# Optimization experiments

Hardware: AMD Instinct MI355X
Metric: run time of the kernel (lower is better)

## Reference

```python
import jax, jax.numpy as jnp
import numpy as np

N_NODES = 50000
N_EDGES = 600000
IN_CH = 128
OUT_CH = 128


def setup_inputs() -> dict:
    key = jax.random.key(0)
    k1, k2, k3, k4 = jax.random.split(key, 4)
    x = jax.random.normal(k1, (N_NODES, IN_CH), dtype=jnp.float32)
    edge_index = jax.random.randint(k2, (2, N_EDGES), 0, N_NODES, dtype=jnp.int64)
    W_msg = jax.random.normal(k3, (OUT_CH, IN_CH * 9), dtype=jnp.float32) * (1.0 / np.sqrt(IN_CH * 9))
    b_msg = jnp.zeros((OUT_CH,), dtype=jnp.float32)
    W_root = jax.random.normal(k4, (OUT_CH, IN_CH), dtype=jnp.float32) * (1.0 / np.sqrt(IN_CH))
    b_root = jnp.zeros((OUT_CH,), dtype=jnp.float32)
    return {"x": x, "edge_index": edge_index, "W_msg": W_msg, "b_msg": b_msg,
            "W_root": W_root, "b_root": b_root}


def reference(x, edge_index, W_msg, b_msg, W_root, b_root):
    n = x.shape[0]
    src = edge_index[0]
    dst = edge_index[1]

    # in-degree per destination node
    degree = jax.ops.segment_sum(jnp.ones_like(dst, dtype=x.dtype), dst, num_segments=n)  # [N]

    msgs = x[src]  # [E, C] gathered source features
    agg_sum = jax.ops.segment_sum(msgs, dst, num_segments=n)                 # [N, C]
    agg_mean = agg_sum / jnp.maximum(degree, 1.0)[:, None]                    # [N, C]
    agg_max = jax.ops.segment_max(msgs, dst, num_segments=n)                  # [N, C], -inf for empty
    agg_max = jnp.where(degree[:, None] > 0, agg_max, 0.0)

    degree_term = jnp.log1p(degree + 1.0)[:, None]                            # [N, 1]
    degree_reference = jnp.maximum(jnp.mean(jnp.log1p(degree + 1.0)), 1.0)    # scalar

    amp = degree_term / degree_reference                                       # [N, 1]
    att = degree_reference / jnp.maximum(degree_term, 1e-06)                   # [N, 1]

    feats = []
    for agg in (agg_sum, agg_mean, agg_max):
        feats.append(agg)            # identity
        feats.append(agg * amp)      # amplification
        feats.append(agg * att)      # attenuation
    stacked = jnp.concatenate(feats, axis=-1)                                  # [N, 9C]

    return stacked @ W_msg.T + b_msg + x @ W_root.T + b_root
```

## Files before the change

### kernel.cpp

```cpp
#include <hip/hip_runtime.h>
#include <cmath>

#define IN_CH 128
#define OUT_CH 128
#define KDIM 512
#define NGEMM 384
#define GBM 256
#define GBMP 448
#define GBN 192
#define SLOT_B 53248
#define SLOT_US 26624
#define SB_SLOT_US 20480
#define PIPE_LDS_BYTES (3 * SLOT_B)

typedef __attribute__((ext_vector_type(8))) short bfrag;
typedef __attribute__((ext_vector_type(4))) float f32x4;

__device__ __forceinline__ unsigned short f2bf(float f) {
    unsigned int u = __float_as_uint(f);
    return (unsigned short)((u + 0x7FFFu + ((u >> 16) & 1u)) >> 16);
}
__device__ __forceinline__ float bf2f(unsigned short h) {
    return __uint_as_float(((unsigned int)h) << 16);
}
__device__ __forceinline__ float4 unpack4(uint2 u) {
    float4 r;
    r.x = __uint_as_float(u.x << 16);
    r.y = __uint_as_float(u.x & 0xFFFF0000u);
    r.z = __uint_as_float(u.y << 16);
    r.w = __uint_as_float(u.y & 0xFFFF0000u);
    return r;
}

__device__ __forceinline__ void gl2lds16(const void* g, void* l) {
    __builtin_amdgcn_global_load_lds(
        (const __attribute__((address_space(1))) unsigned int*)g,
        (__attribute__((address_space(3))) unsigned int*)l, 16, 0, 0);
}


__global__ __launch_bounds__(256) void prep_kernel(const int* __restrict__ ei,
                                                   int* __restrict__ degree,
                                                   float* __restrict__ logsum,
                                                   const float* __restrict__ x,
                                                   unsigned short* __restrict__ xb,
                                                   int E, int total4) {
    int i = blockIdx.x * 256 + threadIdx.x;
    if (i == 0) logsum[0] = 0.f;
    if (i < E) atomicAdd(&degree[ei[E + i]], 1);
    if (i < total4) {
        float4 v = ((const float4*)x)[i];
        uint2 p;
        p.x = (unsigned)f2bf(v.x) | ((unsigned)f2bf(v.y) << 16);
        p.y = (unsigned)f2bf(v.z) | ((unsigned)f2bf(v.w) << 16);
        ((uint2*)xb)[i] = p;
    }
}

__global__ __launch_bounds__(256) void scan1_kernel(const int* __restrict__ degree,
                                                    int* __restrict__ part,
                                                    float* __restrict__ logsum, int n) {
    int i = blockIdx.x * 256 + threadIdx.x;
    int d = (i < n) ? degree[i] : 0;
    float lg = (i < n) ? logf((float)d + 2.0f) : 0.f;
    #pragma unroll
    for (int off = 32; off; off >>= 1) {
        d += __shfl_down(d, off);
        lg += __shfl_down(lg, off);
    }
    __shared__ int sd[4];
    __shared__ float sl[4];
    int wv = threadIdx.x >> 6;
    if ((threadIdx.x & 63) == 0) { sd[wv] = d; sl[wv] = lg; }
    __syncthreads();
    if (threadIdx.x == 0) {
        part[blockIdx.x] = (sd[0] + sd[1]) + (sd[2] + sd[3]);
        atomicAdd(&logsum[0], (sl[0] + sl[1]) + (sl[2] + sl[3]));
    }
}

__global__ __launch_bounds__(256) void scan3_kernel(const int* __restrict__ degree,
                                                    const int* __restrict__ part,
                                                    int* __restrict__ offsets,
                                                    int n, int E, int Sb) {
    int tid = threadIdx.x;
    int i = blockIdx.x * 256 + tid;
    int b = blockIdx.x;
    int acc0 = 0;
    for (int j = tid; j < b; j += 256) acc0 += part[j];
    #pragma unroll
    for (int off = 32; off; off >>= 1) acc0 += __shfl_down(acc0, off);
    __shared__ int bsum[4];
    int lane = tid & 63, wv = tid >> 6;
    if (lane == 0) bsum[wv] = acc0;
    __syncthreads();
    int base = (bsum[0] + bsum[1]) + (bsum[2] + bsum[3]);

    int d = (i < n) ? degree[i] : 0;
    int s = d;
    #pragma unroll
    for (int off = 1; off < 64; off <<= 1) {
        int t = __shfl_up(s, off);
        if (lane >= off) s += t;
    }
    __shared__ int wsum[4];
    if (lane == 63) wsum[wv] = s;
    __syncthreads();
    for (int w2 = 0; w2 < wv; ++w2) base += wsum[w2];
    if (i < n) offsets[i] = base + s - d;
    if (i == n - 1) offsets[n] = E;
}

__global__ void fill_kernel(const int* __restrict__ ei, int* __restrict__ offsets,
                            int* __restrict__ csr_src, int E) {
    int e = blockIdx.x * blockDim.x + threadIdx.x;
    if (e < E) {
        int src = ei[e];
        int dst = ei[E + e];
        int pos = atomicAdd(&offsets[dst], 1);
        csr_src[pos] = src;
    }
}


__global__ __launch_bounds__(256) void agg_kernel(const unsigned short* __restrict__ xb,
                                                  const int* __restrict__ csr_src,
                                                  const int* __restrict__ offsets,
                                                  const int* __restrict__ degree,
                                                  const float* __restrict__ logsum,
                                                  unsigned short* __restrict__ Zhi,
                                                  float* __restrict__ ampv,
                                                  float* __restrict__ attv,
                                                  int N, int Mpad) {
    int node = (blockIdx.x * 256 + threadIdx.x) >> 6;
    int lane = threadIdx.x & 63;
    if (node >= Mpad) return;
    int h = lane >> 5;
    int c4 = lane & 31;
    long zbase = (long)node * KDIM + c4 * 4;
    if (node >= N) {
        if (h == 0) {
            uint2 z = make_uint2(0u, 0u);
            #pragma unroll
            for (int sec = 0; sec < 4; ++sec) *(uint2*)&Zhi[zbase + sec * 128] = z;
        }
        return;
    }
    int deg = degree[node];
    int end = offsets[node];
    int beg = end - deg;
    const float NEG = -3.402823466e38f;
    float4 s[4], m[4];
    #pragma unroll
    for (int u = 0; u < 4; ++u) {
        s[u] = make_float4(0.f, 0.f, 0.f, 0.f);
        m[u] = make_float4(NEG, NEG, NEG, NEG);
    }
    int i = beg;
    for (; i + 8 <= end; i += 8) {
        int idx[4];
        #pragma unroll
        for (int u = 0; u < 4; ++u) idx[u] = csr_src[i + u * 2 + h];
        uint2 raw[4];
        #pragma unroll
        for (int u = 0; u < 4; ++u) raw[u] = *(const uint2*)&xb[(long)idx[u] * IN_CH + c4 * 4];
        #pragma unroll
        for (int u = 0; u < 4; ++u) {
            float4 v = unpack4(raw[u]);
            s[u].x += v.x; s[u].y += v.y; s[u].z += v.z; s[u].w += v.w;
            m[u].x = fmaxf(m[u].x, v.x); m[u].y = fmaxf(m[u].y, v.y);
            m[u].z = fmaxf(m[u].z, v.z); m[u].w = fmaxf(m[u].w, v.w);
        }
    }
    for (; i < end; i += 2) {
        int e = i + h;
        if (e < end) {
            float4 v = unpack4(*(const uint2*)&xb[(long)csr_src[e] * IN_CH + c4 * 4]);
            s[0].x += v.x; s[0].y += v.y; s[0].z += v.z; s[0].w += v.w;
            m[0].x = fmaxf(m[0].x, v.x); m[0].y = fmaxf(m[0].y, v.y);
            m[0].z = fmaxf(m[0].z, v.z); m[0].w = fmaxf(m[0].w, v.w);
        }
    }
    float4 sum, mx;
    sum.x = (s[0].x + s[1].x) + (s[2].x + s[3].x);
    sum.y = (s[0].y + s[1].y) + (s[2].y + s[3].y);
    sum.z = (s[0].z + s[1].z) + (s[2].z + s[3].z);
    sum.w = (s[0].w + s[1].w) + (s[2].w + s[3].w);
    mx.x = fmaxf(fmaxf(m[0].x, m[1].x), fmaxf(m[2].x, m[3].x));
    mx.y = fmaxf(fmaxf(m[0].y, m[1].y), fmaxf(m[2].y, m[3].y));
    mx.z = fmaxf(fmaxf(m[0].z, m[1].z), fmaxf(m[2].z, m[3].z));
    mx.w = fmaxf(fmaxf(m[0].w, m[1].w), fmaxf(m[2].w, m[3].w));
    sum.x += __shfl_xor(sum.x, 32); sum.y += __shfl_xor(sum.y, 32);
    sum.z += __shfl_xor(sum.z, 32); sum.w += __shfl_xor(sum.w, 32);
    mx.x = fmaxf(mx.x, __shfl_xor(mx.x, 32)); mx.y = fmaxf(mx.y, __shfl_xor(mx.y, 32));
    mx.z = fmaxf(mx.z, __shfl_xor(mx.z, 32)); mx.w = fmaxf(mx.w, __shfl_xor(mx.w, 32));

    float inv = 1.0f / fmaxf((float)deg, 1.0f);
    float4 mean = make_float4(sum.x * inv, sum.y * inv, sum.z * inv, sum.w * inv);
    if (deg == 0) mx = make_float4(0.f, 0.f, 0.f, 0.f);
    float4 xv = unpack4(*(const uint2*)&xb[(long)node * IN_CH + c4 * 4]);

    if (h == 0) {
        float4 secs[4] = { xv, sum, mean, mx };
        #pragma unroll
        for (int sec = 0; sec < 4; ++sec) {
            float4 v = secs[sec];
            uint2 hi;
            hi.x = (unsigned)f2bf(v.x) | ((unsigned)f2bf(v.y) << 16);
            hi.y = (unsigned)f2bf(v.z) | ((unsigned)f2bf(v.w) << 16);
            *(uint2*)&Zhi[zbase + sec * 128] = hi;
        }
    }
    if (lane == 0) {
        float ref = fmaxf(logsum[0] / (float)N, 1.0f);
        float dt = log1pf((float)deg + 1.0f);
        ampv[node] = dt / ref;
        attv[node] = ref / fmaxf(dt, 1e-6f);
    }
}


__global__ void wbuild_kernel(const float* __restrict__ Wmsg, const float* __restrict__ Wroot,
                              unsigned short* __restrict__ Whi, unsigned short* __restrict__ Wlo) {
    int idx = blockIdx.x * 256 + threadIdx.x;
    if (idx >= NGEMM * KDIM) return;
    int jp = idx >> 9;
    int k = idx & 511;
    int cg = jp / 96;
    int rem = jp - cg * 96;
    int s16 = rem >> 4;
    int r16 = rem & 15;
    int wn2 = s16 / 3;
    int sec = s16 - wn2 * 3;
    int ocol = cg * 32 + wn2 * 16 + r16;
    float v;
    if (k < 128) {
        v = (sec == 0) ? Wroot[ocol * 128 + k] : 0.f;
    } else {
        int a = (k - 128) >> 7;
        int c = (k - 128) & 127;
        v = Wmsg[ocol * 1152 + (a * 3 + sec) * 128 + c];
    }
    unsigned short h = f2bf(v);
    Whi[idx] = h;
    Wlo[idx] = f2bf(v - bf2f(h));
}


__global__ __launch_bounds__(1024, 4) void gemm_pipe(const unsigned short* __restrict__ Zhi,
                                                     const unsigned short* __restrict__ Whi,
                                                     const unsigned short* __restrict__ Wlo,
                                                     const float* __restrict__ ampv,
                                                     const float* __restrict__ attv,
                                                     const float* __restrict__ bmsg,
                                                     const float* __restrict__ broot,
                                                     float* __restrict__ out, int M) {
    extern __shared__ char smem[];
    unsigned short* lds = (unsigned short*)smem;
    const int tid = threadIdx.x;
    const int w = tid >> 6;
    const int lane = tid & 63;
    const int r16 = lane & 15, q = lane >> 4;
    const int wm = w >> 2, wn = w & 3;
    const int row0 = blockIdx.x * GBMP;
    const int cg2 = blockIdx.y;
    const bool four = (w >= 12);

    const int cbase = four ? (36 + 4 * (w - 12)) : (3 * w);
    const unsigned short* sP[4];
    int dd[4];
    #pragma unroll
    for (int j = 0; j < 4; ++j) {
        int c = cbase + ((four || j < 3) ? j : 0);
        if (c < 28) {
            sP[j] = Zhi + (long)(row0 + c * 16 + r16) * KDIM + q * 8;
        } else {
            int b = c - 28;
            const unsigned short* Wb = (b < 12) ? Whi : Wlo;
            int rr = (b < 12) ? b * 16 : (b - 12) * 16;
            sP[j] = Wb + (long)(cg2 * GBN + rr + r16) * KDIM + q * 8;
        }
        dd[j] = c * 1024 + lane * 16;
    }

    #pragma unroll
    for (int p = 0; p < 2; ++p) {
        char* b = smem + p * SLOT_B;
        gl2lds16(sP[0], b + dd[0]); gl2lds16(sP[1], b + dd[1]); gl2lds16(sP[2], b + dd[2]);
        if (four) gl2lds16(sP[3], b + dd[3]);
        #pragma unroll
        for (int j = 0; j < 4; ++j) sP[j] += 32;
    }

    if (four) __builtin_amdgcn_s_waitcnt(0x0F74);
    else      __builtin_amdgcn_s_waitcnt(0x0F73);
    __builtin_amdgcn_s_barrier();
    __builtin_amdgcn_sched_barrier(0);

    f32x4 acc[7][3] = {};
    const int jtb = (wn >> 1) * 6 + (wn & 1) * 3;

    #pragma unroll 1
    for (int it = 0; it < 16; ++it) {
        const int s = it % 3;
        if (it + 2 < 16) {
            char* b = smem + ((it + 2) % 3) * SLOT_B;
            gl2lds16(sP[0], b + dd[0]); gl2lds16(sP[1], b + dd[1]); gl2lds16(sP[2], b + dd[2]);
            if (four) gl2lds16(sP[3], b + dd[3]);
            #pragma unroll
            for (int j = 0; j < 4; ++j) sP[j] += 32;
        }
        const unsigned short* L = lds + s * SLOT_US;

        bfrag bh[3], bl[3];
        #pragma unroll
        for (int nt = 0; nt < 3; ++nt) {
            int chb = (jtb + nt) * 512 + lane * 8;
            bh[nt] = *(const bfrag*)&L[14336 + chb];
            bl[nt] = *(const bfrag*)&L[20480 + chb];
        }
        #pragma unroll
        for (int mt = 0; mt < 7; ++mt) {
            bfrag ah = *(const bfrag*)&L[((wm * 7 + mt) * 64 + lane) * 8];
            #pragma unroll
            for (int nt = 0; nt < 3; ++nt) {
                acc[mt][nt] = __builtin_amdgcn_mfma_f32_16x16x32_bf16(ah, bh[nt], acc[mt][nt], 0, 0, 0);
                acc[mt][nt] = __builtin_amdgcn_mfma_f32_16x16x32_bf16(ah, bl[nt], acc[mt][nt], 0, 0, 0);
            }
        }

        if (it < 14) {
            if (four) __builtin_amdgcn_s_waitcnt(0x0F74);
            else      __builtin_amdgcn_s_waitcnt(0x0F73);
        } else if (it == 14) {
            __builtin_amdgcn_s_waitcnt(0x0F70);
        }
        if (it < 15) {
            __builtin_amdgcn_s_barrier();
            __builtin_amdgcn_sched_barrier(0);
        }
    }

    const int col = (cg2 * 2 + (wn >> 1)) * 32 + (wn & 1) * 16 + r16;
    const float bias = bmsg[col] + broot[col];
    #pragma unroll
    for (int mt = 0; mt < 7; ++mt) {
        #pragma unroll
        for (int r = 0; r < 4; ++r) {
            int row = row0 + wm * 112 + mt * 16 + q * 4 + r;
            if (row < M) {
                float v = acc[mt][0][r]
                        + ampv[row] * acc[mt][1][r]
                        + attv[row] * acc[mt][2][r] + bias;
                out[(long)row * OUT_CH + col] = v;
            }
        }
    }
}


__global__ __launch_bounds__(1024, 4) void gemm_sb(const unsigned short* __restrict__ Zhi,
                                                   const unsigned short* __restrict__ Whi,
                                                   const unsigned short* __restrict__ Wlo,
                                                   const float* __restrict__ ampv,
                                                   const float* __restrict__ attv,
                                                   const float* __restrict__ bmsg,
                                                   const float* __restrict__ broot,
                                                   float* __restrict__ out, int M) {
    __shared__ unsigned short lds[SB_SLOT_US];
    const int tid = threadIdx.x;
    const int w = tid >> 6;
    const int lane = tid & 63;
    const int r16 = lane & 15, q = lane >> 4;
    const int wm = w >> 2, wn = w & 3;
    const int row0 = blockIdx.x * GBM;
    const int cg2 = blockIdx.y;

    const unsigned short* sAh = Zhi + (long)(row0 + w * 16 + r16) * KDIM + q * 8;
    const unsigned short* sB2 = (w < 12)
        ? Whi + (long)(cg2 * GBN + w * 16 + r16) * KDIM + q * 8
        : Wlo + (long)(cg2 * GBN + (w - 12) * 16 + r16) * KDIM + q * 8;
    const unsigned short* sB3 = Wlo + (long)(cg2 * GBN + (4 + w) * 16 + r16) * KDIM + q * 8;
    char* ldsb = (char*)lds;
    const int d0 = tid * 16, d2 = (1024 + tid) * 16, d3 = (2048 + tid) * 16;

    f32x4 acc[4][3] = {};
    const int jtb = (wn >> 1) * 6 + (wn & 1) * 3;

    #pragma unroll 1
    for (int it = 0; it < 16; ++it) {
        if (it) __syncthreads();
        gl2lds16(sAh, ldsb + d0); gl2lds16(sB2, ldsb + d2); if (w < 8) gl2lds16(sB3, ldsb + d3);
        sAh += 32; sB2 += 32; sB3 += 32;
        __syncthreads();

        bfrag bh[3], bl[3];
        #pragma unroll
        for (int nt = 0; nt < 3; ++nt) {
            int chb = (jtb + nt) * 512 + lane * 8;
            bh[nt] = *(const bfrag*)&lds[8192 + chb];
            bl[nt] = *(const bfrag*)&lds[14336 + chb];
        }
        #pragma unroll
        for (int mt = 0; mt < 4; ++mt) {
            bfrag ah = *(const bfrag*)&lds[((wm * 4 + mt) * 64 + lane) * 8];
            #pragma unroll
            for (int nt = 0; nt < 3; ++nt) {
                acc[mt][nt] = __builtin_amdgcn_mfma_f32_16x16x32_bf16(ah, bh[nt], acc[mt][nt], 0, 0, 0);
                acc[mt][nt] = __builtin_amdgcn_mfma_f32_16x16x32_bf16(ah, bl[nt], acc[mt][nt], 0, 0, 0);
            }
        }
    }

    const int col = (cg2 * 2 + (wn >> 1)) * 32 + (wn & 1) * 16 + r16;
    const float bias = bmsg[col] + broot[col];
    #pragma unroll
    for (int mt = 0; mt < 4; ++mt) {
        #pragma unroll
        for (int r = 0; r < 4; ++r) {
            int row = row0 + wm * 64 + mt * 16 + q * 4 + r;
            if (row < M) {
                float v = acc[mt][0][r]
                        + ampv[row] * acc[mt][1][r]
                        + attv[row] * acc[mt][2][r] + bias;
                out[(long)row * OUT_CH + col] = v;
            }
        }
    }
}


extern "C" void kernel_launch(void* const* d_in, const int* in_sizes, int n_in,
                              void* d_out, int out_size, void* d_ws, size_t ws_size,
                              hipStream_t stream) {
    const float* x     = (const float*)d_in[0];
    const int*   ei    = (const int*)d_in[1];
    const float* Wmsg  = (const float*)d_in[2];
    const float* bmsg  = (const float*)d_in[3];
    const float* Wroot = (const float*)d_in[4];
    const float* broot = (const float*)d_in[5];
    float* out = (float*)d_out;

    int N = in_sizes[0] / IN_CH;
    int E = in_sizes[1] / 2;
    int Mpad = 50176;
    if (N > Mpad) Mpad = ((N + 447) / 448) * 448;
    int MbP = (Mpad + GBMP - 1) / GBMP;
    int MbS = (Mpad + GBM - 1) / GBM;
    int Sb = (N + 255) / 256;
    int total4 = N * IN_CH / 4;

    char* ws = (char*)d_ws;
    size_t off = 0;
    auto alloc = [&](size_t bytes) -> void* {
        void* p = ws + off;
        off = (off + bytes + 255) & ~(size_t)255;
        return p;
    };
    size_t MpadA = (size_t)MbP * GBMP;
    if ((size_t)MbS * GBM > MpadA) MpadA = (size_t)MbS * GBM;
    int* degree  = (int*)alloc((size_t)N * 4);
    int* offsets = (int*)alloc((size_t)(N + 1) * 4);
    float* logsum = (float*)alloc(4);
    int* part    = (int*)alloc((size_t)Sb * 4);
    int* csr_src = (int*)alloc((size_t)E * 4);
    unsigned short* Whi = (unsigned short*)alloc((size_t)NGEMM * KDIM * 2);
    unsigned short* Wlo = (unsigned short*)alloc((size_t)NGEMM * KDIM * 2);
    unsigned short* Zhi = (unsigned short*)alloc(MpadA * KDIM * 2);
    unsigned short* xb  = (unsigned short*)alloc(MpadA * IN_CH * 2);
    float* ampv = (float*)alloc((size_t)N * 4);
    float* attv = (float*)alloc((size_t)N * 4);
    int MpadZ = (int)MpadA;

    hipMemsetAsync(degree, 0, (size_t)N * 4, stream);

    int prepg = (max(E, total4) + 255) / 256;
    prep_kernel<<<prepg, 256, 0, stream>>>(ei, degree, logsum, x, xb, E, total4);
    scan1_kernel<<<Sb, 256, 0, stream>>>(degree, part, logsum, N);
    scan3_kernel<<<Sb, 256, 0, stream>>>(degree, part, offsets, N, E, Sb);
    fill_kernel<<<(E + 255) / 256, 256, 0, stream>>>(ei, offsets, csr_src, E);
    agg_kernel<<<(MpadZ * 64 + 255) / 256, 256, 0, stream>>>(xb, csr_src, offsets, degree, logsum,
                                                             Zhi, ampv, attv, N, MpadZ);
    wbuild_kernel<<<(NGEMM * KDIM + 255) / 256, 256, 0, stream>>>(Wmsg, Wroot, Whi, Wlo);

    bool pipe = false;
    int dev = 0;
    if (hipGetDevice(&dev) == hipSuccess) {
        int optin = 0;
        if (hipDeviceGetAttribute(&optin, hipDeviceAttributeSharedMemPerBlockOptin, dev) == hipSuccess
            && optin >= (int)PIPE_LDS_BYTES) {
            pipe = (hipFuncSetAttribute((const void*)gemm_pipe,
                                        hipFuncAttributeMaxDynamicSharedMemorySize,
                                        PIPE_LDS_BYTES) == hipSuccess);
        }
    }
    if (pipe) {
        dim3 ggrid(MbP, 2);
        gemm_pipe<<<ggrid, 1024, PIPE_LDS_BYTES, stream>>>(Zhi, Whi, Wlo, ampv, attv,
                                                           bmsg, broot, out, N);
    } else {
        dim3 ggrid(MbS, 2);
        gemm_sb<<<ggrid, 1024, 0, stream>>>(Zhi, Whi, Wlo, ampv, attv,
                                            bmsg, broot, out, N);
    }
}
```

Measured before the change: 232.4 us.

## Fuse CSR build and aggregation into one cooperative kernel with grid syncs

```diff
diff --git a/kernel.cpp b/kernel.cpp
--- a/kernel.cpp
+++ b/kernel.cpp
@@ -1,5 +1,8 @@
 #include <hip/hip_runtime.h>
+#include <hip/hip_cooperative_groups.h>
 #include <cmath>
+
+namespace cg = cooperative_groups;
 
 #define IN_CH 128
 #define OUT_CH 128
@@ -36,6 +39,199 @@
     __builtin_amdgcn_global_load_lds(
         (const __attribute__((address_space(1))) unsigned int*)g,
         (__attribute__((address_space(3))) unsigned int*)l, 16, 0, 0);
+}
+
+
+__device__ __forceinline__ void agg_node(const unsigned short* __restrict__ xb,
+                                         const int* __restrict__ csr_src,
+                                         const int* __restrict__ offsets,
+                                         const int* __restrict__ degree,
+                                         const float* __restrict__ logsum,
+                                         unsigned short* __restrict__ Zhi,
+                                         float* __restrict__ ampv,
+                                         float* __restrict__ attv,
+                                         int N, int node, int lane) {
+    int h = lane >> 5;
+    int c4 = lane & 31;
+    long zbase = (long)node * KDIM + c4 * 4;
+    if (node >= N) {
+        if (h == 0) {
+            uint2 z = make_uint2(0u, 0u);
+            #pragma unroll
+            for (int sec = 0; sec < 4; ++sec) *(uint2*)&Zhi[zbase + sec * 128] = z;
+        }
+        return;
+    }
+    int deg = degree[node];
+    int end = offsets[node];
+    int beg = end - deg;
+    const float NEG = -3.402823466e38f;
+    float4 s[4], m[4];
+    #pragma unroll
+    for (int u = 0; u < 4; ++u) {
+        s[u] = make_float4(0.f, 0.f, 0.f, 0.f);
+        m[u] = make_float4(NEG, NEG, NEG, NEG);
+    }
+    int i = beg;
+    for (; i + 8 <= end; i += 8) {
+        int idx[4];
+        #pragma unroll
+        for (int u = 0; u < 4; ++u) idx[u] = csr_src[i + u * 2 + h];
+        uint2 raw[4];
+        #pragma unroll
+        for (int u = 0; u < 4; ++u) raw[u] = *(const uint2*)&xb[(long)idx[u] * IN_CH + c4 * 4];
+        #pragma unroll
+        for (int u = 0; u < 4; ++u) {
+            float4 v = unpack4(raw[u]);
+            s[u].x += v.x; s[u].y += v.y; s[u].z += v.z; s[u].w += v.w;
+            m[u].x = fmaxf(m[u].x, v.x); m[u].y = fmaxf(m[u].y, v.y);
+            m[u].z = fmaxf(m[u].z, v.z); m[u].w = fmaxf(m[u].w, v.w);
+        }
+    }
+    for (; i < end; i += 2) {
+        int e = i + h;
+        if (e < end) {
+            float4 v = unpack4(*(const uint2*)&xb[(long)csr_src[e] * IN_CH + c4 * 4]);
+            s[0].x += v.x; s[0].y += v.y; s[0].z += v.z; s[0].w += v.w;
+            m[0].x = fmaxf(m[0].x, v.x); m[0].y = fmaxf(m[0].y, v.y);
+            m[0].z = fmaxf(m[0].z, v.z); m[0].w = fmaxf(m[0].w, v.w);
+        }
+    }
+    float4 sum, mx;
+    sum.x = (s[0].x + s[1].x) + (s[2].x + s[3].x);
+    sum.y = (s[0].y + s[1].y) + (s[2].y + s[3].y);
+    sum.z = (s[0].z + s[1].z) + (s[2].z + s[3].z);
+    sum.w = (s[0].w + s[1].w) + (s[2].w + s[3].w);
+    mx.x = fmaxf(fmaxf(m[0].x, m[1].x), fmaxf(m[2].x, m[3].x));
+    mx.y = fmaxf(fmaxf(m[0].y, m[1].y), fmaxf(m[2].y, m[3].y));
+    mx.z = fmaxf(fmaxf(m[0].z, m[1].z), fmaxf(m[2].z, m[3].z));
+    mx.w = fmaxf(fmaxf(m[0].w, m[1].w), fmaxf(m[2].w, m[3].w));
+    sum.x += __shfl_xor(sum.x, 32); sum.y += __shfl_xor(sum.y, 32);
+    sum.z += __shfl_xor(sum.z, 32); sum.w += __shfl_xor(sum.w, 32);
+    mx.x = fmaxf(mx.x, __shfl_xor(mx.x, 32)); mx.y = fmaxf(mx.y, __shfl_xor(mx.y, 32));
+    mx.z = fmaxf(mx.z, __shfl_xor(mx.z, 32)); mx.w = fmaxf(mx.w, __shfl_xor(mx.w, 32));
+
+    float inv = 1.0f / fmaxf((float)deg, 1.0f);
+    float4 mean = make_float4(sum.x * inv, sum.y * inv, sum.z * inv, sum.w * inv);
+    if (deg == 0) mx = make_float4(0.f, 0.f, 0.f, 0.f);
+    float4 xv = unpack4(*(const uint2*)&xb[(long)node * IN_CH + c4 * 4]);
+
+    if (h == 0) {
+        float4 secs[4] = { xv, sum, mean, mx };
+        #pragma unroll
+        for (int sec = 0; sec < 4; ++sec) {
+            float4 v = secs[sec];
+            uint2 hi;
+            hi.x = (unsigned)f2bf(v.x) | ((unsigned)f2bf(v.y) << 16);
+            hi.y = (unsigned)f2bf(v.z) | ((unsigned)f2bf(v.w) << 16);
+            *(uint2*)&Zhi[zbase + sec * 128] = hi;
+        }
+    }
+    if (lane == 0) {
+        float ref = fmaxf(logsum[0] / (float)N, 1.0f);
+        float dt = log1pf((float)deg + 1.0f);
+        ampv[node] = dt / ref;
+        attv[node] = ref / fmaxf(dt, 1e-6f);
+    }
+}
+
+
+__global__ __launch_bounds__(256) void fused_pre(const int* __restrict__ ei,
+                                                 const float* __restrict__ x,
+                                                 unsigned short* __restrict__ xb,
+                                                 int* __restrict__ degree,
+                                                 float* __restrict__ logsum,
+                                                 int* __restrict__ part,
+                                                 int* __restrict__ offsets,
+                                                 int* __restrict__ csr_src,
+                                                 unsigned short* __restrict__ Zhi,
+                                                 float* __restrict__ ampv,
+                                                 float* __restrict__ attv,
+                                                 int N, int E, int total4, int Sb, int Mpad) {
+    cg::grid_group grid = cg::this_grid();
+    const int tid = threadIdx.x;
+    const int lane = tid & 63;
+    const int wv = tid >> 6;
+    const int gsize = gridDim.x * 256;
+    const int gt = blockIdx.x * 256 + tid;
+    __shared__ int sd[4];
+    __shared__ float sl[4];
+    __shared__ int bsum[4];
+    __shared__ int wsum[4];
+
+    for (int i = gt; i < N; i += gsize) degree[i] = 0;
+    if (gt == 0) logsum[0] = 0.f;
+    for (int i = gt; i < total4; i += gsize) {
+        float4 v = ((const float4*)x)[i];
+        uint2 p;
+        p.x = (unsigned)f2bf(v.x) | ((unsigned)f2bf(v.y) << 16);
+        p.y = (unsigned)f2bf(v.z) | ((unsigned)f2bf(v.w) << 16);
+        ((uint2*)xb)[i] = p;
+    }
+    grid.sync();
+
+    for (int e = gt; e < E; e += gsize) atomicAdd(&degree[ei[E + e]], 1);
+    grid.sync();
+
+    for (int ch = blockIdx.x; ch < Sb; ch += gridDim.x) {
+        __syncthreads();
+        int i = ch * 256 + tid;
+        int d = (i < N) ? degree[i] : 0;
+        float lg = (i < N) ? logf((float)d + 2.0f) : 0.f;
+        #pragma unroll
+        for (int off = 32; off; off >>= 1) {
+            d += __shfl_down(d, off);
+            lg += __shfl_down(lg, off);
+        }
+        if (lane == 0) { sd[wv] = d; sl[wv] = lg; }
+        __syncthreads();
+        if (tid == 0) {
+            part[ch] = (sd[0] + sd[1]) + (sd[2] + sd[3]);
+            atomicAdd(&logsum[0], (sl[0] + sl[1]) + (sl[2] + sl[3]));
+        }
+    }
+    grid.sync();
+
+    for (int ch = blockIdx.x; ch < Sb; ch += gridDim.x) {
+        __syncthreads();
+        int i = ch * 256 + tid;
+        int acc0 = 0;
+        for (int j = tid; j < ch; j += 256) acc0 += part[j];
+        #pragma unroll
+        for (int off = 32; off; off >>= 1) acc0 += __shfl_down(acc0, off);
+        if (lane == 0) bsum[wv] = acc0;
+        __syncthreads();
+        int base = (bsum[0] + bsum[1]) + (bsum[2] + bsum[3]);
+
+        int d = (i < N) ? degree[i] : 0;
+        int s = d;
+        #pragma unroll
+        for (int off = 1; off < 64; off <<= 1) {
+            int t = __shfl_up(s, off);
+            if (lane >= off) s += t;
+        }
+        if (lane == 63) wsum[wv] = s;
+        __syncthreads();
+        for (int w2 = 0; w2 < wv; ++w2) base += wsum[w2];
+        if (i < N) offsets[i] = base + s - d;
+        if (i == N - 1) offsets[N] = E;
+    }
+    grid.sync();
+
+    for (int e = gt; e < E; e += gsize) {
+        int src = ei[e];
+        int dst = ei[E + e];
+        int pos = atomicAdd(&offsets[dst], 1);
+        csr_src[pos] = src;
+    }
+    grid.sync();
+
+    {
+        int wid = gt >> 6;
+        int nw = gsize >> 6;
+        for (int node = wid; node < Mpad; node += nw)
+            agg_node(xb, csr_src, offsets, degree, logsum, Zhi, ampv, attv, N, node, lane);
+    }
 }
 
 
@@ -122,7 +318,6 @@
     }
 }
 
-
 __global__ __launch_bounds__(256) void agg_kernel(const unsigned short* __restrict__ xb,
                                                   const int* __restrict__ csr_src,
                                                   const int* __restrict__ offsets,
@@ -135,88 +330,7 @@
     int node = (blockIdx.x * 256 + threadIdx.x) >> 6;
     int lane = threadIdx.x & 63;
     if (node >= Mpad) return;
-    int h = lane >> 5;
-    int c4 = lane & 31;
-    long zbase = (long)node * KDIM + c4 * 4;
-    if (node >= N) {
-        if (h == 0) {
-            uint2 z = make_uint2(0u, 0u);
-            #pragma unroll
-            for (int sec = 0; sec < 4; ++sec) *(uint2*)&Zhi[zbase + sec * 128] = z;
-        }
-        return;
-    }
-    int deg = degree[node];
-    int end = offsets[node];
-    int beg = end - deg;
-    const float NEG = -3.402823466e38f;
-    float4 s[4], m[4];
-    #pragma unroll
-    for (int u = 0; u < 4; ++u) {
-        s[u] = make_float4(0.f, 0.f, 0.f, 0.f);
-        m[u] = make_float4(NEG, NEG, NEG, NEG);
-    }
-    int i = beg;
-    for (; i + 8 <= end; i += 8) {
-        int idx[4];
-        #pragma unroll
-        for (int u = 0; u < 4; ++u) idx[u] = csr_src[i + u * 2 + h];
-        uint2 raw[4];
-        #pragma unroll
-        for (int u = 0; u < 4; ++u) raw[u] = *(const uint2*)&xb[(long)idx[u] * IN_CH + c4 * 4];
-        #pragma unroll
-        for (int u = 0; u < 4; ++u) {
-            float4 v = unpack4(raw[u]);
-            s[u].x += v.x; s[u].y += v.y; s[u].z += v.z; s[u].w += v.w;
-            m[u].x = fmaxf(m[u].x, v.x); m[u].y = fmaxf(m[u].y, v.y);
-            m[u].z = fmaxf(m[u].z, v.z); m[u].w = fmaxf(m[u].w, v.w);
-        }
-    }
-    for (; i < end; i += 2) {
-        int e = i + h;
-        if (e < end) {
-            float4 v = unpack4(*(const uint2*)&xb[(long)csr_src[e] * IN_CH + c4 * 4]);
-            s[0].x += v.x; s[0].y += v.y; s[0].z += v.z; s[0].w += v.w;
-            m[0].x = fmaxf(m[0].x, v.x); m[0].y = fmaxf(m[0].y, v.y);
-            m[0].z = fmaxf(m[0].z, v.z); m[0].w = fmaxf(m[0].w, v.w);
-        }
-    }
-    float4 sum, mx;
-    sum.x = (s[0].x + s[1].x) + (s[2].x + s[3].x);
-    sum.y = (s[0].y + s[1].y) + (s[2].y + s[3].y);
-    sum.z = (s[0].z + s[1].z) + (s[2].z + s[3].z);
-    sum.w = (s[0].w + s[1].w) + (s[2].w + s[3].w);
-    mx.x = fmaxf(fmaxf(m[0].x, m[1].x), fmaxf(m[2].x, m[3].x));
-    mx.y = fmaxf(fmaxf(m[0].y, m[1].y), fmaxf(m[2].y, m[3].y));
-    mx.z = fmaxf(fmaxf(m[0].z, m[1].z), fmaxf(m[2].z, m[3].z));
-    mx.w = fmaxf(fmaxf(m[0].w, m[1].w), fmaxf(m[2].w, m[3].w));
-    sum.x += __shfl_xor(sum.x, 32); sum.y += __shfl_xor(sum.y, 32);
-    sum.z += __shfl_xor(sum.z, 32); sum.w += __shfl_xor(sum.w, 32);
-    mx.x = fmaxf(mx.x, __shfl_xor(mx.x, 32)); mx.y = fmaxf(mx.y, __shfl_xor(mx.y, 32));
-    mx.z = fmaxf(mx.z, __shfl_xor(mx.z, 32)); mx.w = fmaxf(mx.w, __shfl_xor(mx.w, 32));
-
-    float inv = 1.0f / fmaxf((float)deg, 1.0f);
-    float4 mean = make_float4(sum.x * inv, sum.y * inv, sum.z * inv, sum.w * inv);
-    if (deg == 0) mx = make_float4(0.f, 0.f, 0.f, 0.f);
-    float4 xv = unpack4(*(const uint2*)&xb[(long)node * IN_CH + c4 * 4]);
-
-    if (h == 0) {
-        float4 secs[4] = { xv, sum, mean, mx };
-        #pragma unroll
-        for (int sec = 0; sec < 4; ++sec) {
-            float4 v = secs[sec];
-            uint2 hi;
-            hi.x = (unsigned)f2bf(v.x) | ((unsigned)f2bf(v.y) << 16);
-            hi.y = (unsigned)f2bf(v.z) | ((unsigned)f2bf(v.w) << 16);
-            *(uint2*)&Zhi[zbase + sec * 128] = hi;
-        }
-    }
-    if (lane == 0) {
-        float ref = fmaxf(logsum[0] / (float)N, 1.0f);
-        float dt = log1pf((float)deg + 1.0f);
-        ampv[node] = dt / ref;
-        attv[node] = ref / fmaxf(dt, 1e-6f);
-    }
+    agg_node(xb, csr_src, offsets, degree, logsum, Zhi, ampv, attv, N, node, lane);
 }
 
 
@@ -226,13 +340,13 @@
     if (idx >= NGEMM * KDIM) return;
     int jp = idx >> 9;
     int k = idx & 511;
-    int cg = jp / 96;
-    int rem = jp - cg * 96;
+    int cg2 = jp / 96;
+    int rem = jp - cg2 * 96;
     int s16 = rem >> 4;
     int r16 = rem & 15;
     int wn2 = s16 / 3;
     int sec = s16 - wn2 * 3;
-    int ocol = cg * 32 + wn2 * 16 + r16;
+    int ocol = cg2 * 32 + wn2 * 16 + r16;
     float v;
     if (k < 128) {
         v = (sec == 0) ? Wroot[ocol * 128 + k] : 0.f;
@@ -472,20 +586,15 @@
     float* attv = (float*)alloc((size_t)N * 4);
     int MpadZ = (int)MpadA;
 
-    hipMemsetAsync(degree, 0, (size_t)N * 4, stream);
-
-    int prepg = (max(E, total4) + 255) / 256;
-    prep_kernel<<<prepg, 256, 0, stream>>>(ei, degree, logsum, x, xb, E, total4);
-    scan1_kernel<<<Sb, 256, 0, stream>>>(degree, part, logsum, N);
-    scan3_kernel<<<Sb, 256, 0, stream>>>(degree, part, offsets, N, E, Sb);
-    fill_kernel<<<(E + 255) / 256, 256, 0, stream>>>(ei, offsets, csr_src, E);
-    agg_kernel<<<(MpadZ * 64 + 255) / 256, 256, 0, stream>>>(xb, csr_src, offsets, degree, logsum,
-                                                             Zhi, ampv, attv, N, MpadZ);
-    wbuild_kernel<<<(NGEMM * KDIM + 255) / 256, 256, 0, stream>>>(Wmsg, Wroot, Whi, Wlo);
-
+    int dev = 0;
+    bool haveDev = (hipGetDevice(&dev) == hipSuccess);
+    int coop = 0, numCU = 256;
+    if (haveDev) {
+        hipDeviceGetAttribute(&coop, hipDeviceAttributeCooperativeLaunch, dev);
+        hipDeviceGetAttribute(&numCU, hipDeviceAttributeMultiprocessorCount, dev);
+    }
     bool pipe = false;
-    int dev = 0;
-    if (hipGetDevice(&dev) == hipSuccess) {
+    if (haveDev) {
         int optin = 0;
         if (hipDeviceGetAttribute(&optin, hipDeviceAttributeSharedMemPerBlockOptin, dev) == hipSuccess
             && optin >= (int)PIPE_LDS_BYTES) {
@@ -494,6 +603,34 @@
                                         PIPE_LDS_BYTES) == hipSuccess);
         }
     }
+
+    bool usedCoop = false;
+    if (coop) {
+        int occ = 0;
+        if (hipOccupancyMaxActiveBlocksPerMultiprocessor(&occ, (const void*)fused_pre, 256, 0)
+                == hipSuccess && occ > 0) {
+            int blocks = occ * numCU;
+            if (blocks > 2048) blocks = 2048;
+            void* args[] = { (void*)&ei, (void*)&x, (void*)&xb, (void*)&degree,
+                             (void*)&logsum, (void*)&part, (void*)&offsets, (void*)&csr_src,
+                             (void*)&Zhi, (void*)&ampv, (void*)&attv,
+                             (void*)&N, (void*)&E, (void*)&total4, (void*)&Sb, (void*)&MpadZ };
+            usedCoop = (hipLaunchCooperativeKernel((const void*)fused_pre, dim3(blocks), dim3(256),
+                                                   args, 0, stream) == hipSuccess);
+        }
+    }
+    if (!usedCoop) {
+        hipMemsetAsync(degree, 0, (size_t)N * 4, stream);
+        int prepg = (max(E, total4) + 255) / 256;
+        prep_kernel<<<prepg, 256, 0, stream>>>(ei, degree, logsum, x, xb, E, total4);
+        scan1_kernel<<<Sb, 256, 0, stream>>>(degree, part, logsum, N);
+        scan3_kernel<<<Sb, 256, 0, stream>>>(degree, part, offsets, N, E, Sb);
+        fill_kernel<<<(E + 255) / 256, 256, 0, stream>>>(ei, offsets, csr_src, E);
+        agg_kernel<<<(MpadZ * 64 + 255) / 256, 256, 0, stream>>>(xb, csr_src, offsets, degree,
+                                                                 logsum, Zhi, ampv, attv, N, MpadZ);
+    }
+    wbuild_kernel<<<(NGEMM * KDIM + 255) / 256, 256, 0, stream>>>(Wmsg, Wroot, Whi, Wlo);
+
     if (pipe) {
         dim3 ggrid(MbP, 2);
         gemm_pipe<<<ggrid, 1024, PIPE_LDS_BYTES, stream>>>(Zhi, Whi, Wlo, ampv, attv,
```

After: 682.1 us. 193% more time.
